# Optimization experiments

Hardware: AMD Instinct MI355X
Metric: run time of the kernel (lower is better)

Reference implementation:

```python
import jax, jax.numpy as jnp
import numpy as np

HEADS = 16

def _rotate_half(t):
    t1, t2 = jnp.split(t, 2, axis=-1)
    return jnp.concatenate([-t2, t1], axis=-1)

def _apply_rope(q, k, sin, cos):
    # sin/cos: [Lp, hd] -> broadcast to [1,1,Lp,hd]
    sin = sin[None, None, :, :]
    cos = cos[None, None, :, :]
    q = q * cos + _rotate_half(q) * sin
    k = k * cos + _rotate_half(k) * sin
    return q, k

def setup_inputs() -> dict:
    key = jax.random.key(0)
    ks = jax.random.split(key, 6)
    B, L, C = 16, 1025, 1024
    hd = C // HEADS
    x = jax.random.normal(ks[0], (B, L, C), dtype=jnp.float32)
    sin = jax.random.uniform(ks[1], (L - 1, hd), dtype=jnp.float32)
    cos = jax.random.uniform(ks[2], (L - 1, hd), dtype=jnp.float32)
    qkv_w = jax.random.normal(ks[3], (3 * C, C), dtype=jnp.float32) * 0.02
    proj_w = jax.random.normal(ks[4], (C, C), dtype=jnp.float32) * 0.02
    proj_b = jnp.zeros((C,), dtype=jnp.float32)
    return {"x": x, "sin": sin, "cos": cos, "qkv_w": qkv_w, "proj_w": proj_w, "proj_b": proj_b}

def reference(x, sin, cos, qkv_w, proj_w, proj_b):
    B, L, C = x.shape
    H = HEADS
    hd = C // H
    scale = hd ** (-0.5)
    # QKV projection (no bias), split into heads: [3, B, H, L, hd]
    qkv = (x @ qkv_w.T).reshape(B, L, 3, H, hd).transpose(2, 0, 3, 1, 4)
    q, k, v = qkv[0], qkv[1], qkv[2]
    # L == sin.shape[0] + 1 -> CLS token split, RoPE on patch tokens only
    q_cls, q_patch = q[:, :, :1], q[:, :, 1:]
    k_cls, k_patch = k[:, :, :1], k[:, :, 1:]
    q_patch, k_patch = _apply_rope(q_patch, k_patch, sin, cos)
    q = jnp.concatenate([q_cls, q_patch], axis=2)
    k = jnp.concatenate([k_cls, k_patch], axis=2)
    attn = jnp.einsum("bhqd,bhkd->bhqk", q, k) * scale
    attn = jax.nn.softmax(attn, axis=-1)
    out = jnp.einsum("bhqk,bhkd->bhqd", attn, v)  # [B,H,L,hd]
    out = out.transpose(0, 2, 1, 3).reshape(B, L, C)
    return out @ proj_w.T + proj_b
```

## Files before the change

kernel.cpp:

```cpp
#include <hip/hip_runtime.h>

typedef unsigned short ushort_t;
typedef unsigned int uint_t;
typedef __attribute__((ext_vector_type(8))) short short8;
typedef __attribute__((ext_vector_type(4))) float f32x4;

#define Bv 16
#define Lv 1025
#define LpD 1088
#define Cv 1024
#define Hv 16
#define BHv 256
#define Mv 16400
#define Mp 16512

#define MFMA(a, b, c) __builtin_amdgcn_mfma_f32_16x16x32_bf16(a, b, c, 0, 0, 0)

__device__ __forceinline__ ushort_t f2b(float x) {
    uint_t u = __float_as_uint(x);
    u = (u + 0x7FFFu + ((u >> 16) & 1u)) >> 16;
    return (ushort_t)u;
}
__device__ __forceinline__ float b2f(ushort_t v) {
    return __uint_as_float(((uint_t)v) << 16);
}
__device__ __forceinline__ uint_t pk2(float a, float b) {
#if __has_builtin(__builtin_amdgcn_cvt_pk_bf16_f32)
    typedef __attribute__((ext_vector_type(2))) __bf16 bf16x2;
    bf16x2 r = __builtin_amdgcn_cvt_pk_bf16_f32(a, b);
    return *(uint_t*)&r;
#else
    return (uint_t)f2b(a) | ((uint_t)f2b(b) << 16);
#endif
}

__device__ __forceinline__ void gl2lds16(const ushort_t* g, void* lds) {
    __builtin_amdgcn_global_load_lds(
        (const __attribute__((address_space(1))) void*)g,
        (__attribute__((address_space(3))) void*)lds, 16, 0, 0);
}

__device__ __forceinline__ short8 frag(const ushort_t* base, int row, int chunk) {
    return *(const short8*)(base + row * 64 + ((chunk ^ (row & 7)) << 3));
}

__global__ __launch_bounds__(256) void conv_bf16(const float* __restrict__ s,
                                                 ushort_t* __restrict__ d,
                                                 int n_valid, int n_total) {
    int i = (blockIdx.x * 256 + threadIdx.x) * 4;
    if (i >= n_total) return;
    float4 v = make_float4(0.f, 0.f, 0.f, 0.f);
    if (i < n_valid) v = *(const float4*)(s + i);
    ushort4 o;
    o.x = f2b(v.x); o.y = f2b(v.y); o.z = f2b(v.z); o.w = f2b(v.w);
    *(ushort4*)(d + i) = o;
}

__global__ __launch_bounds__(256, 4) void gemm_qkv(const ushort_t* __restrict__ A,
                                                   const ushort_t* __restrict__ W,
                                                   ushort_t* __restrict__ Q,
                                                   ushort_t* __restrict__ K,
                                                   ushort_t* __restrict__ V,
                                                   const float* __restrict__ sinp,
                                                   const float* __restrict__ cosp) {
    __shared__ uint4 sm[2112];
    ushort_t* As = (ushort_t*)sm;
    ushort_t* Bs = As + 128 * 64;
    const int t = threadIdx.x;
    const int w = t >> 6, l = t & 63;
    const int m0 = blockIdx.y * 128, n0 = blockIdx.x * 128;
    const int wm = (w >> 1) * 64, wn = (w & 1) * 64;
    const int srow = (w * 32) + (l >> 3);
    const int scs = (l & 7) ^ (srow & 7);
    f32x4 acc[4][4] = {};
    for (int k0 = 0; k0 < 1024; k0 += 64) {
        __syncthreads();
#pragma unroll
        for (int i = 0; i < 4; i++) {
            int row = srow + i * 8;
            gl2lds16(A + (size_t)(m0 + row) * 1024 + k0 + scs * 8,
                     As + (w * 32 + i * 8) * 64);
            gl2lds16(W + (size_t)(n0 + row) * 1024 + k0 + scs * 8,
                     Bs + (w * 32 + i * 8) * 64);
        }
        __syncthreads();
#pragma unroll
        for (int kb = 0; kb < 2; kb++) {
            short8 af[4], bf[4];
#pragma unroll
            for (int mb = 0; mb < 4; mb++)
                af[mb] = frag(As, wm + mb * 16 + (l & 15), kb * 4 + (l >> 4));
#pragma unroll
            for (int nb = 0; nb < 4; nb++)
                bf[nb] = frag(Bs, wn + nb * 16 + (l & 15), kb * 4 + (l >> 4));
#pragma unroll
            for (int mb = 0; mb < 4; mb++)
#pragma unroll
                for (int nb = 0; nb < 4; nb++)
                    acc[mb][nb] = MFMA(af[mb], bf[nb], acc[mb][nb]);
        }
    }
    __syncthreads();
    ushort_t (*St)[132] = (ushort_t(*)[132])sm;
#pragma unroll
    for (int mb = 0; mb < 4; mb++)
#pragma unroll
        for (int r = 0; r < 4; r++)
#pragma unroll
            for (int nb = 0; nb < 4; nb++)
                St[wm + mb * 16 + (l >> 4) * 4 + r][wn + nb * 16 + (l & 15)] =
                    f2b(acc[mb][nb][r]);
    __syncthreads();
#pragma unroll
    for (int it = 0; it < 8; it++) {
        int seg = it * 32 + w * 8 + (l >> 3);
        int mr = seg >> 1, p = seg & 1;
        int m = m0 + mr;
        if (m >= Mv) continue;
        int b = m / 1025, lseq = m - b * 1025;
        int n = n0 + p * 64;
        int which = n >> 10, h = (n >> 6) & 15;
        ushort_t* dst = (which == 0) ? Q : ((which == 1) ? K : V);
        const int d0 = (l & 7) * 8;
        size_t doff = ((size_t)(b * Hv + h) * LpD + lseq) * 64 + d0;
        if (which <= 1 && lseq > 0) {
            const ushort_t* rowp = &St[mr][p * 64];
            const float* cw = cosp + (lseq - 1) * 64 + d0;
            const float* sw = sinp + (lseq - 1) * 64 + d0;
            float4 c0 = *(const float4*)cw, c1 = *(const float4*)(cw + 4);
            float4 s0 = *(const float4*)sw, s1 = *(const float4*)(sw + 4);
            float cc[8] = {c0.x, c0.y, c0.z, c0.w, c1.x, c1.y, c1.z, c1.w};
            float ss[8] = {s0.x, s0.y, s0.z, s0.w, s1.x, s1.y, s1.z, s1.w};
            float sgn = (d0 < 32) ? -1.f : 1.f;
            uint_t ov[4];
#pragma unroll
            for (int jj = 0; jj < 4; jj++) {
                float f0 = b2f(rowp[d0 + jj * 2]);
                float f1 = b2f(rowp[d0 + jj * 2 + 1]);
                float r0 = b2f(rowp[(d0 ^ 32) + jj * 2]) * sgn;
                float r1 = b2f(rowp[(d0 ^ 32) + jj * 2 + 1]) * sgn;
                ov[jj] = pk2(f0 * cc[jj * 2] + r0 * ss[jj * 2],
                             f1 * cc[jj * 2 + 1] + r1 * ss[jj * 2 + 1]);
            }
            *(uint4*)(dst + doff) = *(uint4*)ov;
        } else {
            *(uint4*)(dst + doff) = *(const uint4*)&St[mr][p * 64 + d0];
        }
    }
}

__global__ __launch_bounds__(256) void transpose_v(const ushort_t* __restrict__ Vb,
                                                   ushort_t* __restrict__ Vt) {
    __shared__ ushort_t Ts[64][72];
    const int t = threadIdx.x;
    const int l0 = blockIdx.x * 64, bh = blockIdx.y;
#pragma unroll
    for (int i = 0; i < 2; i++) {
        int c = t + 256 * i; int row = c >> 3, cir = c & 7;
        *(uint4*)&Ts[row][cir * 8] =
            *(const uint4*)(Vb + ((size_t)bh * LpD + l0 + row) * 64 + cir * 8);
    }
    __syncthreads();
#pragma unroll
    for (int i = 0; i < 2; i++) {
        int c = t + 256 * i; int d = c >> 3, lg = c & 7;
        short8 v;
#pragma unroll
        for (int j = 0; j < 8; j++) v[j] = (short)Ts[lg * 8 + j][d];
        *(short8*)(Vt + ((size_t)bh * 64 + d) * LpD + l0 + lg * 8) = v;
    }
}

__global__ __launch_bounds__(256, 3) void attn_mfma(const ushort_t* __restrict__ Qb,
                                                    const ushort_t* __restrict__ Kb,
                                                    const ushort_t* __restrict__ Vt,
                                                    ushort_t* __restrict__ AO) {
    __shared__ ushort_t Qs[64 * 64];
    __shared__ ushort_t Kd[2][64 * 64];
    __shared__ ushort_t Vd[2][64 * 64];
    __shared__ ushort_t Ps[64][72];
    const int t = threadIdx.x, w = t >> 6, l = t & 63;
    const int qt = blockIdx.x, bh = blockIdx.y;
    const int q0 = qt * 64;
    const size_t kbase = (size_t)bh * LpD * 64;
    const size_t vbase = (size_t)bh * 64 * LpD;
    const int scs = (l & 7) ^ ((l >> 3) & 7);

#pragma unroll
    for (int i = 0; i < 2; i++) {
        int row = w * 16 + i * 8 + (l >> 3);
        gl2lds16(Qb + kbase + (size_t)(q0 + row) * 64 + scs * 8,
                 Qs + (w * 16 + i * 8) * 64);
    }
#pragma unroll
    for (int i = 0; i < 2; i++) {
        int row = w * 16 + i * 8 + (l >> 3);
        gl2lds16(Kb + kbase + (size_t)row * 64 + scs * 8,
                 Kd[0] + (w * 16 + i * 8) * 64);
        gl2lds16(Vt + vbase + (size_t)row * LpD + scs * 8,
                 Vd[0] + (w * 16 + i * 8) * 64);
    }
    asm volatile("s_waitcnt vmcnt(4)" ::: "memory");
    asm volatile("s_barrier" ::: "memory");
    short8 aq0 = frag(Qs, w * 16 + (l & 15), l >> 4);
    short8 aq1 = frag(Qs, w * 16 + (l & 15), 4 + (l >> 4));

    short8 ones;
#pragma unroll
    for (int j = 0; j < 8; j++) ones[j] = (short)0x3F80;
    f32x4 o[4] = {};
    f32x4 sacc = {};
    const float CE = 0.18033688011112042f;

    for (int kt = 0; kt < 17; kt++) {
        const ushort_t* Ks = Kd[kt & 1];
        const ushort_t* Vs = Vd[kt & 1];
        if (kt < 16) {
#pragma unroll
            for (int i = 0; i < 2; i++) {
                int row = w * 16 + i * 8 + (l >> 3);
                gl2lds16(Kb + kbase + (size_t)((kt + 1) * 64 + row) * 64 + scs * 8,
                         Kd[(kt + 1) & 1] + (w * 16 + i * 8) * 64);
                gl2lds16(Vt + vbase + (size_t)row * LpD + (kt + 1) * 64 + scs * 8,
                         Vd[(kt + 1) & 1] + (w * 16 + i * 8) * 64);
            }
            asm volatile("s_waitcnt vmcnt(4)" ::: "memory");
        } else {
            asm volatile("s_waitcnt vmcnt(0)" ::: "memory");
        }
        asm volatile("s_barrier" ::: "memory");
#pragma unroll
        for (int cb = 0; cb < 4; cb++) {
            short8 bk0 = frag(Ks, cb * 16 + (l & 15), l >> 4);
            short8 bk1 = frag(Ks, cb * 16 + (l & 15), 4 + (l >> 4));
            f32x4 s = {};
            s = MFMA(aq0, bk0, s);
            s = MFMA(aq1, bk1, s);
            float p4[4];
#pragma unroll
            for (int r = 0; r < 4; r++) p4[r] = exp2f(s[r] * CE);
            if (kt == 16) {
                int key = 1024 + cb * 16 + (l & 15);
                if (key >= Lv) { p4[0] = p4[1] = p4[2] = p4[3] = 0.f; }
            }
            uint_t pk01 = pk2(p4[0], p4[1]);
            uint_t pk23 = pk2(p4[2], p4[3]);
            ushort_t* pr = &Ps[w * 16 + (l >> 4) * 4][cb * 16 + (l & 15)];
            pr[0 * 72] = (ushort_t)pk01;
            pr[1 * 72] = (ushort_t)(pk01 >> 16);
            pr[2 * 72] = (ushort_t)pk23;
            pr[3 * 72] = (ushort_t)(pk23 >> 16);
        }
        short8 ap0 = *(const short8*)&Ps[w * 16 + (l & 15)][(l >> 4) * 8];
        short8 ap1 = *(const short8*)&Ps[w * 16 + (l & 15)][32 + (l >> 4) * 8];
        __builtin_amdgcn_s_setprio(1);
        sacc = MFMA(ap0, ones, sacc);
        sacc = MFMA(ap1, ones, sacc);
#pragma unroll
        for (int cb = 0; cb < 4; cb++) {
            short8 bv0 = frag(Vs, cb * 16 + (l & 15), l >> 4);
            short8 bv1 = frag(Vs, cb * 16 + (l & 15), 4 + (l >> 4));
            o[cb] = MFMA(ap0, bv0, o[cb]);
            o[cb] = MFMA(ap1, bv1, o[cb]);
        }
        __builtin_amdgcn_s_setprio(0);
        asm volatile("s_barrier" ::: "memory");
    }
    const int b = bh >> 4, h = bh & 15;
#pragma unroll
    for (int r = 0; r < 4; r++) {
        int lq = q0 + w * 16 + (l >> 4) * 4 + r;
        if (lq >= Lv) continue;
        float inv = 1.f / sacc[r];
        size_t ob = ((size_t)(b * 1025 + lq)) * 1024 + h * 64;
#pragma unroll
        for (int cb = 0; cb < 4; cb++)
            AO[ob + cb * 16 + (l & 15)] = f2b(o[cb][r] * inv);
    }
}

__global__ __launch_bounds__(256, 4) void gemm_proj(const ushort_t* __restrict__ A,
                                                    const ushort_t* __restrict__ W,
                                                    const float* __restrict__ bias,
                                                    float* __restrict__ out) {
    __shared__ uint4 sm[2112];
    ushort_t* As = (ushort_t*)sm;
    ushort_t* Bs = As + 128 * 64;
    const int t = threadIdx.x;
    const int w = t >> 6, l = t & 63;
    const int m0 = blockIdx.y * 128, n0 = blockIdx.x * 128;
    const int wm = (w >> 1) * 64, wn = (w & 1) * 64;
    const int srow = (w * 32) + (l >> 3);
    const int scs = (l & 7) ^ (srow & 7);
    f32x4 acc[4][4] = {};
    for (int k0 = 0; k0 < 1024; k0 += 64) {
        __syncthreads();
#pragma unroll
        for (int i = 0; i < 4; i++) {
            int row = srow + i * 8;
            gl2lds16(A + (size_t)(m0 + row) * 1024 + k0 + scs * 8,
                     As + (w * 32 + i * 8) * 64);
            gl2lds16(W + (size_t)(n0 + row) * 1024 + k0 + scs * 8,
                     Bs + (w * 32 + i * 8) * 64);
        }
        __syncthreads();
#pragma unroll
        for (int kb = 0; kb < 2; kb++) {
            short8 af[4], bf[4];
#pragma unroll
            for (int mb = 0; mb < 4; mb++)
                af[mb] = frag(As, wm + mb * 16 + (l & 15), kb * 4 + (l >> 4));
#pragma unroll
            for (int nb = 0; nb < 4; nb++)
                bf[nb] = frag(Bs, wn + nb * 16 + (l & 15), kb * 4 + (l >> 4));
#pragma unroll
            for (int mb = 0; mb < 4; mb++)
#pragma unroll
                for (int nb = 0; nb < 4; nb++)
                    acc[mb][nb] = MFMA(af[mb], bf[nb], acc[mb][nb]);
        }
    }
    float bias4[4];
#pragma unroll
    for (int nb = 0; nb < 4; nb++) bias4[nb] = bias[n0 + wn + nb * 16 + (l & 15)];
    float (*Sf)[132] = (float(*)[132])sm;
#pragma unroll
    for (int half = 0; half < 2; half++) {
        __syncthreads();
        if ((w >> 1) == half) {
#pragma unroll
            for (int mb = 0; mb < 4; mb++)
#pragma unroll
                for (int r = 0; r < 4; r++)
#pragma unroll
                    for (int nb = 0; nb < 4; nb++)
                        Sf[mb * 16 + (l >> 4) * 4 + r][wn + nb * 16 + (l & 15)] =
                            acc[mb][nb][r] + bias4[nb];
        }
        __syncthreads();
#pragma unroll
        for (int it = 0; it < 8; it++) {
            int rr = it * 8 + w * 2 + (l >> 5);
            int m = m0 + half * 64 + rr;
            if (m < Mv)
                *(float4*)(out + (size_t)m * 1024 + n0 + (l & 31) * 4) =
                    *(const float4*)&Sf[rr][(l & 31) * 4];
        }
    }
}

extern "C" void kernel_launch(void* const* d_in, const int* in_sizes, int n_in,
                              void* d_out, int out_size, void* d_ws, size_t ws_size,
                              hipStream_t stream) {
    (void)in_sizes; (void)n_in; (void)out_size; (void)ws_size;
    const float* x      = (const float*)d_in[0];
    const float* sinp   = (const float*)d_in[1];
    const float* cosp   = (const float*)d_in[2];
    const float* qkv_w  = (const float*)d_in[3];
    const float* proj_w = (const float*)d_in[4];
    const float* proj_b = (const float*)d_in[5];
    float* out = (float*)d_out;

    const size_t SZH = (size_t)BHv * LpD * 64;
    ushort_t* xb  = (ushort_t*)d_ws;
    ushort_t* qwb = xb + (size_t)Mp * 1024;
    ushort_t* pwb = qwb + (size_t)3072 * 1024;
    ushort_t* Qb  = pwb + (size_t)1024 * 1024;
    ushort_t* Kb  = Qb + SZH;
    ushort_t* Vb  = Kb + SZH;
    ushort_t* Vt  = Vb + SZH;
    ushort_t* AO  = Vt + SZH;

    dim3 blk(256);
    conv_bf16<<<dim3(Mp * 1024 / 1024), blk, 0, stream>>>(x, xb, Mv * 1024, Mp * 1024);
    conv_bf16<<<dim3(3072 * 1024 / 1024), blk, 0, stream>>>(qkv_w, qwb, 3072 * 1024, 3072 * 1024);
    conv_bf16<<<dim3(1024 * 1024 / 1024), blk, 0, stream>>>(proj_w, pwb, 1024 * 1024, 1024 * 1024);
    gemm_qkv<<<dim3(24, 129), blk, 0, stream>>>(xb, qwb, Qb, Kb, Vb, sinp, cosp);
    transpose_v<<<dim3(17, BHv), blk, 0, stream>>>(Vb, Vt);
    attn_mfma<<<dim3(17, BHv), blk, 0, stream>>>(Qb, Kb, Vt, AO);
    gemm_proj<<<dim3(8, 129), blk, 0, stream>>>(AO, pwb, proj_b, out);
}
```

Baseline: 488.8 us.

## Compute transposed scores and reuse Q LDS buffer for P to raise attention occupancy

```diff
diff --git a/kernel.cpp b/kernel.cpp
--- a/kernel.cpp
+++ b/kernel.cpp
@@ -171,26 +171,28 @@
     }
 }
 
-__global__ __launch_bounds__(256, 3) void attn_mfma(const ushort_t* __restrict__ Qb,
+__global__ __launch_bounds__(256, 4) void attn_mfma(const ushort_t* __restrict__ Qb,
                                                     const ushort_t* __restrict__ Kb,
                                                     const ushort_t* __restrict__ Vt,
                                                     ushort_t* __restrict__ AO) {
-    __shared__ ushort_t Qs[64 * 64];
+    __shared__ ushort_t QP[64 * 64];
     __shared__ ushort_t Kd[2][64 * 64];
     __shared__ ushort_t Vd[2][64 * 64];
-    __shared__ ushort_t Ps[64][72];
     const int t = threadIdx.x, w = t >> 6, l = t & 63;
     const int qt = blockIdx.x, bh = blockIdx.y;
     const int q0 = qt * 64;
     const size_t kbase = (size_t)bh * LpD * 64;
     const size_t vbase = (size_t)bh * 64 * LpD;
     const int scs = (l & 7) ^ ((l >> 3) & 7);
+    const int g = l >> 4;
+    const int qr = l & 15;
+    const int q7 = l & 7;
 
 #pragma unroll
     for (int i = 0; i < 2; i++) {
         int row = w * 16 + i * 8 + (l >> 3);
         gl2lds16(Qb + kbase + (size_t)(q0 + row) * 64 + scs * 8,
-                 Qs + (w * 16 + i * 8) * 64);
+                 QP + (w * 16 + i * 8) * 64);
     }
 #pragma unroll
     for (int i = 0; i < 2; i++) {
@@ -202,8 +204,11 @@
     }
     asm volatile("s_waitcnt vmcnt(4)" ::: "memory");
     asm volatile("s_barrier" ::: "memory");
-    short8 aq0 = frag(Qs, w * 16 + (l & 15), l >> 4);
-    short8 aq1 = frag(Qs, w * 16 + (l & 15), 4 + (l >> 4));
+    short8 aq0 = frag(QP, w * 16 + qr, g);
+    short8 aq1 = frag(QP, w * 16 + qr, 4 + g);
+    asm volatile("s_waitcnt lgkmcnt(0)" ::: "memory");
+
+    ushort_t* prow = QP + (w * 16 + qr) * 64;
 
     short8 ones;
 #pragma unroll
@@ -231,35 +236,33 @@
         asm volatile("s_barrier" ::: "memory");
 #pragma unroll
         for (int cb = 0; cb < 4; cb++) {
-            short8 bk0 = frag(Ks, cb * 16 + (l & 15), l >> 4);
-            short8 bk1 = frag(Ks, cb * 16 + (l & 15), 4 + (l >> 4));
+            short8 bk0 = frag(Ks, cb * 16 + qr, g);
+            short8 bk1 = frag(Ks, cb * 16 + qr, 4 + g);
             f32x4 s = {};
-            s = MFMA(aq0, bk0, s);
-            s = MFMA(aq1, bk1, s);
+            s = MFMA(bk0, aq0, s);
+            s = MFMA(bk1, aq1, s);
             float p4[4];
 #pragma unroll
             for (int r = 0; r < 4; r++) p4[r] = exp2f(s[r] * CE);
             if (kt == 16) {
-                int key = 1024 + cb * 16 + (l & 15);
-                if (key >= Lv) { p4[0] = p4[1] = p4[2] = p4[3] = 0.f; }
+                bool keep0 = (cb == 0) && (g == 0);
+                p4[0] = keep0 ? p4[0] : 0.f;
+                p4[1] = 0.f; p4[2] = 0.f; p4[3] = 0.f;
             }
-            uint_t pk01 = pk2(p4[0], p4[1]);
-            uint_t pk23 = pk2(p4[2], p4[3]);
-            ushort_t* pr = &Ps[w * 16 + (l >> 4) * 4][cb * 16 + (l & 15)];
-            pr[0 * 72] = (ushort_t)pk01;
-            pr[1 * 72] = (ushort_t)(pk01 >> 16);
-            pr[2 * 72] = (ushort_t)pk23;
-            pr[3 * 72] = (ushort_t)(pk23 >> 16);
-        }
-        short8 ap0 = *(const short8*)&Ps[w * 16 + (l & 15)][(l >> 4) * 8];
-        short8 ap1 = *(const short8*)&Ps[w * 16 + (l & 15)][32 + (l >> 4) * 8];
+            uint2 pw;
+            pw.x = pk2(p4[0], p4[1]);
+            pw.y = pk2(p4[2], p4[3]);
+            *(uint2*)(prow + (((2 * cb + (g >> 1)) ^ q7) << 3) + ((g & 1) << 2)) = pw;
+        }
+        short8 ap0 = *(const short8*)(prow + ((g ^ q7) << 3));
+        short8 ap1 = *(const short8*)(prow + (((4 + g) ^ q7) << 3));
         __builtin_amdgcn_s_setprio(1);
         sacc = MFMA(ap0, ones, sacc);
         sacc = MFMA(ap1, ones, sacc);
 #pragma unroll
         for (int cb = 0; cb < 4; cb++) {
-            short8 bv0 = frag(Vs, cb * 16 + (l & 15), l >> 4);
-            short8 bv1 = frag(Vs, cb * 16 + (l & 15), 4 + (l >> 4));
+            short8 bv0 = frag(Vs, cb * 16 + qr, g);
+            short8 bv1 = frag(Vs, cb * 16 + qr, 4 + g);
             o[cb] = MFMA(ap0, bv0, o[cb]);
             o[cb] = MFMA(ap1, bv1, o[cb]);
         }
@@ -269,13 +272,13 @@
     const int b = bh >> 4, h = bh & 15;
 #pragma unroll
     for (int r = 0; r < 4; r++) {
-        int lq = q0 + w * 16 + (l >> 4) * 4 + r;
+        int lq = q0 + w * 16 + g * 4 + r;
         if (lq >= Lv) continue;
         float inv = 1.f / sacc[r];
         size_t ob = ((size_t)(b * 1025 + lq)) * 1024 + h * 64;
 #pragma unroll
         for (int cb = 0; cb < 4; cb++)
-            AO[ob + cb * 16 + (l & 15)] = f2b(o[cb][r] * inv);
+            AO[ob + cb * 16 + qr] = f2b(o[cb][r] * inv);
     }
 }
 
```

After: 487.3 us. Within noise of the previous version (-0.3%).
